# Optimization experiments

Hardware: AMD Instinct MI355X
Metric: run time of the kernel (lower is better)

## Reference

```python
import jax, jax.numpy as jnp
import numpy as np

# dims: batch B, tokens T, model_dim D, expert hidden H, experts E, top-k K
B, T, D, H, E, K = 4, 2048, 2048, 2048, 8, 2
CAP_FACTOR = 1.0
S = B * T
C = int(np.ceil(K * S / E * CAP_FACTOR))  # per-expert capacity = 2048


def setup_inputs() -> dict:
    key = jax.random.key(0)
    k0, k1, k2, k3 = jax.random.split(key, 4)
    x = jax.random.normal(k0, (B, T, D), dtype=jnp.float32)
    wg = jax.random.normal(k1, (D, E), dtype=jnp.float32) * (D ** -0.5)
    w1 = jax.random.normal(k2, (E, D, H), dtype=jnp.float32) * (D ** -0.5)
    b1 = jnp.zeros((E, H), dtype=jnp.float32)
    w2 = jax.random.normal(k3, (E, H, D), dtype=jnp.float32) * (H ** -0.5)
    b2 = jnp.zeros((E, D), dtype=jnp.float32)
    return {"x": x, "wg": wg, "w1": w1, "b1": b1, "w2": w2, "b2": b2}


def _moe(x, wg, w1, b1, w2, b2):
    xt = x.reshape(S, D)
    # --- top-k gating (deepspeed-style, gates normalized over selected k) ---
    gates = jax.nn.softmax(xt @ wg, axis=-1)            # [S,E]
    vals, idx = jax.lax.top_k(gates, K)                 # [S,K]
    vals = vals / jnp.sum(vals, axis=-1, keepdims=True)
    # --- capacity-aware slot assignment (slot j offset by counts of slots < j) ---
    m = jax.nn.one_hot(idx, E, dtype=jnp.int32).transpose(1, 0, 2)  # [K,S,E]
    within = jnp.cumsum(m, axis=1) - m                  # 0-based rank within expert per slot
    counts = jnp.sum(m, axis=1)                         # [K,E]
    offs = jnp.cumsum(counts, axis=0) - counts          # [K,E] offsets from earlier slots
    loc = jnp.sum((within + offs[:, None, :]) * m, axis=2)  # [K,S]
    eid = idx.T                                         # [K,S]
    valid = loc < C
    loc_c = jnp.minimum(loc, C - 1)
    # --- dispatch: scatter raw tokens into [E,C,D] expert buffers ---
    contrib = jnp.where(valid[..., None], xt[None, :, :], 0.0)   # [K,S,D]
    disp = jnp.zeros((E, C, D), x.dtype).at[eid, loc_c].add(contrib)
    # --- grouped expert FFN: relu(x @ W1 + b1) @ W2 + b2 ---
    h = jax.nn.relu(jnp.einsum('ecd,edh->ech', disp, w1) + b1[:, None, :])
    ye = jnp.einsum('ech,ehd->ecd', h, w2) + b2[:, None, :]
    # --- combine: gather expert outputs, weight by normalized gates ---
    gathered = ye[eid, loc_c]                           # [K,S,D]
    w = (vals.T * valid).astype(x.dtype)                # [K,S]
    out = jnp.einsum('ks,ksd->sd', w, gathered)
    return out.reshape(B, T, D)


def reference(x, wg, w1, b1, w2, b2):
    y = _moe(x, wg, w1, b1, w2, b2)                     # [B,T,D]
    return jax.nn.log_softmax(jnp.sum(y, axis=2), axis=1)  # [B,T]
```

## Files before the change

### kernel.cpp

```cpp
#include <hip/hip_runtime.h>
#include <math.h>

#define S_TOK 8192
#define DDIM 2048
#define HDIM 2048
#define NE 8
#define CAP 2048
#define NBATCH 4
#define TT 2048

typedef _Float16 f16;
typedef _Float16 f16x4 __attribute__((ext_vector_type(4)));
typedef _Float16 f16x8 __attribute__((ext_vector_type(8)));
typedef float f32x4 __attribute__((ext_vector_type(4)));

__global__ __launch_bounds__(256) void gating_kernel(const float* __restrict__ x,
                                                     const float* __restrict__ wg,
                                                     int* __restrict__ eid,
                                                     float* __restrict__ wts) {
  int wid = threadIdx.x >> 6;
  int lane = threadIdx.x & 63;
  int s = blockIdx.x * 4 + wid;
  const float4* x4 = (const float4*)x;
  const float4* wg4 = (const float4*)wg;
  double acc[8];
#pragma unroll
  for (int e = 0; e < 8; ++e) acc[e] = 0.0;
  for (int j = 0; j < 8; ++j) {
    int v = j * 64 + lane;
    float4 xv = x4[(size_t)s * 512 + v];
    const float4* wp = wg4 + (size_t)(v * 4) * 2;
#pragma unroll
    for (int ii = 0; ii < 4; ++ii) {
      float xs = (ii == 0) ? xv.x : (ii == 1) ? xv.y : (ii == 2) ? xv.z : xv.w;
      float4 g0 = wp[ii * 2];
      float4 g1 = wp[ii * 2 + 1];
      double xd = (double)xs;
      acc[0] += xd * (double)g0.x; acc[1] += xd * (double)g0.y;
      acc[2] += xd * (double)g0.z; acc[3] += xd * (double)g0.w;
      acc[4] += xd * (double)g1.x; acc[5] += xd * (double)g1.y;
      acc[6] += xd * (double)g1.z; acc[7] += xd * (double)g1.w;
    }
  }
#pragma unroll
  for (int e = 0; e < 8; ++e) {
    double v = acc[e];
    for (int off = 32; off > 0; off >>= 1) v += __shfl_down(v, off, 64);
    acc[e] = v;
  }
  if (lane == 0) {
    int e0 = 0; double l0 = acc[0];
    for (int e = 1; e < 8; ++e) if (acc[e] > l0) { l0 = acc[e]; e0 = e; }
    int e1 = -1; double l1 = -1e300;
    for (int e = 0; e < 8; ++e) if (e != e0 && acc[e] > l1) { l1 = acc[e]; e1 = e; }
    double pe = exp(l1 - l0);
    double inv = 1.0 / (1.0 + pe);
    eid[2 * s] = e0; eid[2 * s + 1] = e1;
    wts[2 * s] = (float)inv; wts[2 * s + 1] = (float)(pe * inv);
  }
}

__global__ __launch_bounds__(256) void w2s_kernel(const float* __restrict__ w2,
                                                  float* __restrict__ w2s) {
  int wid = threadIdx.x >> 6, lane = threadIdx.x & 63;
  int row = blockIdx.x * 4 + wid;
  const float4* w24 = (const float4*)w2;
  float acc = 0.f;
  for (int j = 0; j < 8; ++j) {
    float4 v = w24[(size_t)row * 512 + j * 64 + lane];
    acc += v.x + v.y + v.z + v.w;
  }
  for (int off = 32; off > 0; off >>= 1) acc += __shfl_down(acc, off, 64);
  if (lane == 0) w2s[row] = acc;
}

__global__ __launch_bounds__(64) void b2s_kernel(const float* __restrict__ b2,
                                                 float* __restrict__ b2s) {
  int e = blockIdx.x; int lane = threadIdx.x;
  float acc = 0.f;
  for (int j = 0; j < 32; ++j) acc += b2[e * 2048 + j * 64 + lane];
  for (int off = 32; off > 0; off >>= 1) acc += __shfl_down(acc, off, 64);
  if (lane == 0) b2s[e] = acc;
}

__global__ __launch_bounds__(256) void scan_kernel(const int* __restrict__ eid,
                                                   int* __restrict__ locb,
                                                   int* __restrict__ slot_token) {
  __shared__ int baseLds[2][8];
  __shared__ int wcnt[2][4][8];
  __shared__ int c0tmp[8];
  int tid = threadIdx.x, wid = tid >> 6, lane = tid & 63;
  if (tid < 8) c0tmp[tid] = 0;
  __syncthreads();
  {
    int cnt = 0;
    for (int r = 0; r < 32; ++r) {
      int s = r * 256 + tid;
      int e0 = eid[2 * s];
#pragma unroll
      for (int e = 0; e < 8; ++e) {
        unsigned long long bal = __ballot(e0 == e);
        if (lane == e) cnt += __popcll(bal);
      }
    }
    if (lane < 8) atomicAdd(&c0tmp[lane], cnt);
  }
  __syncthreads();
  if (tid < 8) { baseLds[0][tid] = 0; baseLds[1][tid] = c0tmp[tid]; }
  __syncthreads();
  unsigned long long lower = (lane == 0) ? 0ull : ((~0ull) >> (64 - lane));
  for (int r = 0; r < 32; ++r) {
    int s = r * 256 + tid;
    int e0 = eid[2 * s], e1 = eid[2 * s + 1];
    int rank0 = 0, rank1 = 0;
#pragma unroll
    for (int e = 0; e < 8; ++e) {
      unsigned long long bal0 = __ballot(e0 == e);
      unsigned long long bal1 = __ballot(e1 == e);
      if (e0 == e) rank0 = __popcll(bal0 & lower);
      if (e1 == e) rank1 = __popcll(bal1 & lower);
      if (lane == e) { wcnt[0][wid][e] = __popcll(bal0); wcnt[1][wid][e] = __popcll(bal1); }
    }
    __syncthreads();
    int loc0 = baseLds[0][e0] + rank0;
    int loc1 = baseLds[1][e1] + rank1;
    for (int w = 0; w < wid; ++w) { loc0 += wcnt[0][w][e0]; loc1 += wcnt[1][w][e1]; }
    locb[2 * s] = loc0; locb[2 * s + 1] = loc1;
    if (loc0 < CAP) slot_token[e0 * CAP + loc0] = s;
    if (loc1 < CAP) slot_token[e1 * CAP + loc1] = s;
    __syncthreads();
    if (tid < 16) {
      int k = tid >> 3, e = tid & 7;
      baseLds[k][e] += wcnt[k][0][e] + wcnt[k][1][e] + wcnt[k][2][e] + wcnt[k][3][e];
    }
    __syncthreads();
  }
}

__global__ __launch_bounds__(256) void abuild_kernel(const float* __restrict__ x,
                                                     const int* __restrict__ slot_token,
                                                     f16* __restrict__ A16) {
  int slot = blockIdx.x;
  int s = slot_token[slot];
  const float4* x4 = (const float4*)x + (size_t)s * 512;
  f16x4* out = (f16x4*)(A16 + (size_t)slot * DDIM);
#pragma unroll
  for (int i = 0; i < 2; ++i) {
    int v = i * 256 + threadIdx.x;
    float4 xv = x4[v];
    f16x4 h;
    h[0] = (f16)xv.x; h[1] = (f16)xv.y; h[2] = (f16)xv.z; h[3] = (f16)xv.w;
    out[v] = h;
  }
}

__global__ __launch_bounds__(256) void w1t_kernel(const float* __restrict__ w1,
                                                  f16* __restrict__ W1T) {
  __shared__ f16 tile[64 * 68];
  int b = blockIdx.x;
  int e = b >> 10; int rem = b & 1023;
  int d0 = (rem >> 5) << 6;
  int h0 = (rem & 31) << 6;
  const float4* src = (const float4*)w1;
#pragma unroll
  for (int i = 0; i < 4; ++i) {
    int linear = i * 256 + threadIdx.x;
    int r = linear >> 4, c4 = linear & 15;
    float4 v = src[((size_t)e * DDIM * HDIM + (size_t)(d0 + r) * HDIM + h0) / 4 + c4];
    int tb = r * 68 + c4 * 4;
    tile[tb + 0] = (f16)v.x; tile[tb + 1] = (f16)v.y;
    tile[tb + 2] = (f16)v.z; tile[tb + 3] = (f16)v.w;
  }
  __syncthreads();
#pragma unroll
  for (int i = 0; i < 4; ++i) {
    int linear = i * 256 + threadIdx.x;
    int hr = linear >> 4, dc4 = linear & 15;
    f16x4 o;
    o[0] = tile[(dc4 * 4 + 0) * 68 + hr];
    o[1] = tile[(dc4 * 4 + 1) * 68 + hr];
    o[2] = tile[(dc4 * 4 + 2) * 68 + hr];
    o[3] = tile[(dc4 * 4 + 3) * 68 + hr];
    *(f16x4*)(W1T + (size_t)e * HDIM * DDIM + (size_t)(h0 + hr) * DDIM + d0 + dc4 * 4) = o;
  }
}

__global__ __launch_bounds__(256) void gemm_kernel(const f16* __restrict__ A16,
                                                   const f16* __restrict__ W1T,
                                                   const float* __restrict__ b1,
                                                   const float* __restrict__ w2s,
                                                   float* __restrict__ zacc) {
  __shared__ __align__(16) f16 As[128 * 32];
  __shared__ __align__(16) f16 Bs[128 * 32];
  int tid = threadIdx.x;
  int wid = tid >> 6, lane = tid & 63;
  int cT = blockIdx.x, hT = blockIdx.y, e = blockIdx.z;
  int c0 = cT * 128, h0 = hT * 128;
  const f16* Abase = A16 + ((size_t)e * CAP + c0) * DDIM;
  const f16* Bbase = W1T + ((size_t)e * HDIM + h0) * DDIM;
  f32x4 acc[4][4];
#pragma unroll
  for (int i = 0; i < 4; ++i)
#pragma unroll
    for (int j = 0; j < 4; ++j) acc[i][j] = (f32x4){0.f, 0.f, 0.f, 0.f};
  int wm = (wid >> 1) * 64, wn = (wid & 1) * 64;
  int quad = lane >> 4, l15 = lane & 15;

  for (int k0 = 0; k0 < DDIM; k0 += 32) {
    __syncthreads();
#pragma unroll
    for (int i = 0; i < 2; ++i) {
      int off = (i * 256 + tid) * 8;
      int row = off >> 5, col = off & 31;
      *(uint4*)&As[off] = *(const uint4*)&Abase[(size_t)row * DDIM + k0 + col];
      *(uint4*)&Bs[off] = *(const uint4*)&Bbase[(size_t)row * DDIM + k0 + col];
    }
    __syncthreads();
    f16x8 af[4], bfr[4];
#pragma unroll
    for (int mt = 0; mt < 4; ++mt)
      af[mt] = *(const f16x8*)&As[(wm + mt * 16 + l15) * 32 + quad * 8];
#pragma unroll
    for (int nt = 0; nt < 4; ++nt)
      bfr[nt] = *(const f16x8*)&Bs[(wn + nt * 16 + l15) * 32 + quad * 8];
#pragma unroll
    for (int mt = 0; mt < 4; ++mt)
#pragma unroll
      for (int nt = 0; nt < 4; ++nt)
        acc[mt][nt] = __builtin_amdgcn_mfma_f32_16x16x32_f16(af[mt], bfr[nt], acc[mt][nt], 0, 0, 0);
  }
  float b1v[4], wsv[4];
#pragma unroll
  for (int nt = 0; nt < 4; ++nt) {
    int h = h0 + wn + nt * 16 + l15;
    b1v[nt] = b1[e * HDIM + h];
    wsv[nt] = w2s[e * HDIM + h];
  }
#pragma unroll
  for (int mt = 0; mt < 4; ++mt) {
    float pr[4];
#pragma unroll
    for (int r = 0; r < 4; ++r) {
      float t = 0.f;
#pragma unroll
      for (int nt = 0; nt < 4; ++nt) {
        float v = acc[mt][nt][r] + b1v[nt];
        t += (v > 0.f ? v : 0.f) * wsv[nt];
      }
      pr[r] = t;
    }
#pragma unroll
    for (int r = 0; r < 4; ++r)
#pragma unroll
      for (int off = 1; off < 16; off <<= 1) pr[r] += __shfl_xor(pr[r], off, 64);
    if (l15 == 0) {
      int m = c0 + wm + mt * 16 + quad * 4;
#pragma unroll
      for (int r = 0; r < 4; ++r) atomicAdd(&zacc[e * CAP + m + r], pr[r]);
    }
  }
}

__global__ __launch_bounds__(256) void combine_kernel(const int* __restrict__ eid,
                                                      const int* __restrict__ locb,
                                                      const float* __restrict__ wts,
                                                      const float* __restrict__ zacc,
                                                      const float* __restrict__ b2s,
                                                      float* __restrict__ z) {
  int s = blockIdx.x * 256 + threadIdx.x;
  float zz = 0.f;
#pragma unroll
  for (int k = 0; k < 2; ++k) {
    int e = eid[2 * s + k], loc = locb[2 * s + k];
    if (loc < CAP) zz += wts[2 * s + k] * (zacc[e * CAP + loc] + b2s[e]);
  }
  z[s] = zz;
}

__global__ __launch_bounds__(256) void lsm_kernel(const float* __restrict__ z,
                                                  float* __restrict__ out) {
  __shared__ float red[4];
  int b = blockIdx.x, tid = threadIdx.x;
  int wid = tid >> 6, lane = tid & 63;
  const float* zr = z + b * TT;
  float v[8];
  float mx = -1e30f;
#pragma unroll
  for (int i = 0; i < 8; ++i) { v[i] = zr[i * 256 + tid]; mx = fmaxf(mx, v[i]); }
  for (int off = 32; off > 0; off >>= 1) mx = fmaxf(mx, __shfl_xor(mx, off, 64));
  if (lane == 0) red[wid] = mx;
  __syncthreads();
  mx = fmaxf(fmaxf(red[0], red[1]), fmaxf(red[2], red[3]));
  float sum = 0.f;
#pragma unroll
  for (int i = 0; i < 8; ++i) sum += expf(v[i] - mx);
  for (int off = 32; off > 0; off >>= 1) sum += __shfl_xor(sum, off, 64);
  __syncthreads();
  if (lane == 0) red[wid] = sum;
  __syncthreads();
  sum = red[0] + red[1] + red[2] + red[3];
  float lse = mx + logf(sum);
#pragma unroll
  for (int i = 0; i < 8; ++i) out[b * TT + i * 256 + tid] = v[i] - lse;
}

extern "C" void kernel_launch(void* const* d_in, const int* in_sizes, int n_in,
                              void* d_out, int out_size, void* d_ws, size_t ws_size,
                              hipStream_t stream) {
  const float* x  = (const float*)d_in[0];
  const float* wg = (const float*)d_in[1];
  const float* w1 = (const float*)d_in[2];
  const float* b1 = (const float*)d_in[3];
  const float* w2 = (const float*)d_in[4];
  const float* b2 = (const float*)d_in[5];
  float* out = (float*)d_out;

  char* ws = (char*)d_ws;
  size_t off = 0;
  auto alloc = [&](size_t bytes) -> char* {
    char* p = ws + off;
    off += (bytes + 255) & ~(size_t)255;
    return p;
  };
  f16* A16 = (f16*)alloc((size_t)NE * CAP * DDIM * 2);
  f16* W1T = (f16*)alloc((size_t)NE * HDIM * DDIM * 2);
  float* w2s = (float*)alloc((size_t)NE * HDIM * 4);
  float* b2s = (float*)alloc(NE * 4);
  int* eid = (int*)alloc((size_t)S_TOK * 2 * 4);
  float* wts = (float*)alloc((size_t)S_TOK * 2 * 4);
  int* locb = (int*)alloc((size_t)S_TOK * 2 * 4);
  int* slot_token = (int*)alloc((size_t)NE * CAP * 4);
  float* zacc = (float*)alloc((size_t)NE * CAP * 4);
  float* z = (float*)alloc((size_t)S_TOK * 4);
  if (off > ws_size) return;

  hipMemsetAsync(slot_token, 0, NE * CAP * 4, stream);
  hipMemsetAsync(zacc, 0, NE * CAP * 4, stream);

  gating_kernel<<<S_TOK / 4, 256, 0, stream>>>(x, wg, eid, wts);
  w2s_kernel<<<NE * HDIM / 4, 256, 0, stream>>>(w2, w2s);
  b2s_kernel<<<NE, 64, 0, stream>>>(b2, b2s);
  scan_kernel<<<1, 256, 0, stream>>>(eid, locb, slot_token);
  abuild_kernel<<<NE * CAP, 256, 0, stream>>>(x, slot_token, A16);
  w1t_kernel<<<NE * 32 * 32, 256, 0, stream>>>(w1, W1T);
  gemm_kernel<<<dim3(CAP / 128, HDIM / 128, NE), 256, 0, stream>>>(A16, W1T, b1, w2s, zacc);
  combine_kernel<<<S_TOK / 256, 256, 0, stream>>>(eid, locb, wts, zacc, b2s, z);
  lsm_kernel<<<NBATCH, 256, 0, stream>>>(z, out);
}
```

Before: 650.7 us.

## Fuse prep kernels, drop memsets, use direct global-to-LDS loads in GEMM

Folds the workspace zeroing into the gating kernel and merges w1 transpose, w2/b2 row sums and the A16 build into a single prep launch. Combine and log-softmax are fused into one tail kernel. The GEMM now stages tiles with global_load_lds, bypassing registers, and remaps block IDs into 4x4 groups for L2 reuse. The w1 transpose tile is kept in fp32 with 8-wide f16 stores. This cuts launch count and staging overhead, but puts several unrelated changes together and leans on the direct-to-LDS builtin's layout matching the fragment reads.

```diff
diff --git a/kernel.cpp b/kernel.cpp
--- a/kernel.cpp
+++ b/kernel.cpp
@@ -14,10 +14,20 @@
 typedef _Float16 f16x8 __attribute__((ext_vector_type(8)));
 typedef float f32x4 __attribute__((ext_vector_type(4)));
 
+typedef __attribute__((address_space(1))) const void* gas_ptr;
+typedef __attribute__((address_space(3))) void* las_ptr;
+
 __global__ __launch_bounds__(256) void gating_kernel(const float* __restrict__ x,
                                                      const float* __restrict__ wg,
                                                      int* __restrict__ eid,
-                                                     float* __restrict__ wts) {
+                                                     float* __restrict__ wts,
+                                                     int* __restrict__ slot_token,
+                                                     float* __restrict__ zacc) {
+  if (blockIdx.x < 64) {
+    int i = blockIdx.x * 256 + threadIdx.x;
+    slot_token[i] = 0;
+    zacc[i] = 0.f;
+  }
   int wid = threadIdx.x >> 6;
   int lane = threadIdx.x & 63;
   int s = blockIdx.x * 4 + wid;
@@ -60,29 +70,6 @@
   }
 }
 
-__global__ __launch_bounds__(256) void w2s_kernel(const float* __restrict__ w2,
-                                                  float* __restrict__ w2s) {
-  int wid = threadIdx.x >> 6, lane = threadIdx.x & 63;
-  int row = blockIdx.x * 4 + wid;
-  const float4* w24 = (const float4*)w2;
-  float acc = 0.f;
-  for (int j = 0; j < 8; ++j) {
-    float4 v = w24[(size_t)row * 512 + j * 64 + lane];
-    acc += v.x + v.y + v.z + v.w;
-  }
-  for (int off = 32; off > 0; off >>= 1) acc += __shfl_down(acc, off, 64);
-  if (lane == 0) w2s[row] = acc;
-}
-
-__global__ __launch_bounds__(64) void b2s_kernel(const float* __restrict__ b2,
-                                                 float* __restrict__ b2s) {
-  int e = blockIdx.x; int lane = threadIdx.x;
-  float acc = 0.f;
-  for (int j = 0; j < 32; ++j) acc += b2[e * 2048 + j * 64 + lane];
-  for (int off = 32; off > 0; off >>= 1) acc += __shfl_down(acc, off, 64);
-  if (lane == 0) b2s[e] = acc;
-}
-
 __global__ __launch_bounds__(256) void scan_kernel(const int* __restrict__ eid,
                                                    int* __restrict__ locb,
                                                    int* __restrict__ slot_token) {
@@ -137,51 +124,80 @@
   }
 }
 
-__global__ __launch_bounds__(256) void abuild_kernel(const float* __restrict__ x,
-                                                     const int* __restrict__ slot_token,
-                                                     f16* __restrict__ A16) {
-  int slot = blockIdx.x;
-  int s = slot_token[slot];
-  const float4* x4 = (const float4*)x + (size_t)s * 512;
-  f16x4* out = (f16x4*)(A16 + (size_t)slot * DDIM);
-#pragma unroll
-  for (int i = 0; i < 2; ++i) {
-    int v = i * 256 + threadIdx.x;
-    float4 xv = x4[v];
-    f16x4 h;
-    h[0] = (f16)xv.x; h[1] = (f16)xv.y; h[2] = (f16)xv.z; h[3] = (f16)xv.w;
-    out[v] = h;
-  }
-}
-
-__global__ __launch_bounds__(256) void w1t_kernel(const float* __restrict__ w1,
-                                                  f16* __restrict__ W1T) {
-  __shared__ f16 tile[64 * 68];
-  int b = blockIdx.x;
-  int e = b >> 10; int rem = b & 1023;
-  int d0 = (rem >> 5) << 6;
-  int h0 = (rem & 31) << 6;
-  const float4* src = (const float4*)w1;
-#pragma unroll
-  for (int i = 0; i < 4; ++i) {
-    int linear = i * 256 + threadIdx.x;
-    int r = linear >> 4, c4 = linear & 15;
-    float4 v = src[((size_t)e * DDIM * HDIM + (size_t)(d0 + r) * HDIM + h0) / 4 + c4];
-    int tb = r * 68 + c4 * 4;
-    tile[tb + 0] = (f16)v.x; tile[tb + 1] = (f16)v.y;
-    tile[tb + 2] = (f16)v.z; tile[tb + 3] = (f16)v.w;
-  }
-  __syncthreads();
-#pragma unroll
-  for (int i = 0; i < 4; ++i) {
-    int linear = i * 256 + threadIdx.x;
-    int hr = linear >> 4, dc4 = linear & 15;
-    f16x4 o;
-    o[0] = tile[(dc4 * 4 + 0) * 68 + hr];
-    o[1] = tile[(dc4 * 4 + 1) * 68 + hr];
-    o[2] = tile[(dc4 * 4 + 2) * 68 + hr];
-    o[3] = tile[(dc4 * 4 + 3) * 68 + hr];
-    *(f16x4*)(W1T + (size_t)e * HDIM * DDIM + (size_t)(h0 + hr) * DDIM + d0 + dc4 * 4) = o;
+#define W1T_BLOCKS 8192
+#define W2S_BLOCKS 4096
+#define ABUILD_BASE (W1T_BLOCKS + W2S_BLOCKS + 1)
+__global__ __launch_bounds__(256) void prep_kernel(const float* __restrict__ w1,
+                                                   const float* __restrict__ w2,
+                                                   const float* __restrict__ b2,
+                                                   const float* __restrict__ x,
+                                                   const int* __restrict__ slot_token,
+                                                   f16* __restrict__ W1T,
+                                                   float* __restrict__ w2s,
+                                                   float* __restrict__ b2s,
+                                                   f16* __restrict__ A16) {
+  __shared__ float tile[64 * 65];
+  int bid = blockIdx.x, tid = threadIdx.x;
+  if (bid >= ABUILD_BASE) {
+    int slot = bid - ABUILD_BASE;
+    int s = slot_token[slot];
+    const float4* x4 = (const float4*)x + (size_t)s * 512;
+    f16x4* outp = (f16x4*)(A16 + (size_t)slot * DDIM);
+#pragma unroll
+    for (int i = 0; i < 2; ++i) {
+      int v = i * 256 + tid;
+      float4 xv = x4[v];
+      f16x4 h;
+      h[0] = (f16)xv.x; h[1] = (f16)xv.y; h[2] = (f16)xv.z; h[3] = (f16)xv.w;
+      outp[v] = h;
+    }
+    return;
+  }
+  if (bid < W1T_BLOCKS) {
+    int e = bid >> 10, rem = bid & 1023;
+    int d0 = (rem >> 5) << 6;
+    int h0 = (rem & 31) << 6;
+    const float* w1e = w1 + (size_t)e * DDIM * HDIM;
+#pragma unroll
+    for (int i = 0; i < 4; ++i) {
+      int linear = i * 256 + tid;
+      int r = linear >> 4, c4 = linear & 15;
+      float4 v = *(const float4*)(w1e + (size_t)(d0 + r) * HDIM + h0 + c4 * 4);
+      float* t = &tile[r * 65 + c4 * 4];
+      t[0] = v.x; t[1] = v.y; t[2] = v.z; t[3] = v.w;
+    }
+    __syncthreads();
+    f16* W1Te = W1T + (size_t)e * HDIM * DDIM;
+#pragma unroll
+    for (int i = 0; i < 2; ++i) {
+      int linear = i * 256 + tid;
+      int hr = linear >> 3, l8 = linear & 7;
+      f16x8 o;
+#pragma unroll
+      for (int j = 0; j < 8; ++j) o[j] = (f16)tile[(l8 * 8 + j) * 65 + hr];
+      *(f16x8*)(W1Te + (size_t)(h0 + hr) * DDIM + d0 + l8 * 8) = o;
+    }
+    return;
+  }
+  if (bid < W1T_BLOCKS + W2S_BLOCKS) {
+    int wid = tid >> 6, lane = tid & 63;
+    int row = (bid - W1T_BLOCKS) * 4 + wid;
+    const float4* w24 = (const float4*)w2;
+    float acc = 0.f;
+    for (int j = 0; j < 8; ++j) {
+      float4 v = w24[(size_t)row * 512 + j * 64 + lane];
+      acc += v.x + v.y + v.z + v.w;
+    }
+    for (int off = 32; off > 0; off >>= 1) acc += __shfl_down(acc, off, 64);
+    if (lane == 0) w2s[row] = acc;
+    return;
+  }
+  {
+    int e = tid >> 5, l32 = tid & 31;
+    float acc = 0.f;
+    for (int j = 0; j < 64; ++j) acc += b2[e * 2048 + j * 32 + l32];
+    for (int off = 16; off > 0; off >>= 1) acc += __shfl_down(acc, off, 32);
+    if (l32 == 0) b2s[e] = acc;
   }
 }
 
@@ -194,7 +210,12 @@
   __shared__ __align__(16) f16 Bs[128 * 32];
   int tid = threadIdx.x;
   int wid = tid >> 6, lane = tid & 63;
-  int cT = blockIdx.x, hT = blockIdx.y, e = blockIdx.z;
+  int bid = blockIdx.x;
+  int e = bid >> 8;
+  int r = bid & 255;
+  int st = r >> 4, wi = r & 15;
+  int cT = (st >> 2) * 4 + (wi >> 2);
+  int hT = (st & 3) * 4 + (wi & 3);
   int c0 = cT * 128, h0 = hT * 128;
   const f16* Abase = A16 + ((size_t)e * CAP + c0) * DDIM;
   const f16* Bbase = W1T + ((size_t)e * HDIM + h0) * DDIM;
@@ -206,15 +227,19 @@
   int wm = (wid >> 1) * 64, wn = (wid & 1) * 64;
   int quad = lane >> 4, l15 = lane & 15;
 
+  const f16* Aln = Abase + (size_t)(wid * 32 + (lane >> 2)) * DDIM + (lane & 3) * 8;
+  const f16* Bln = Bbase + (size_t)(wid * 32 + (lane >> 2)) * DDIM + (lane & 3) * 8;
+  f16* ldsA0 = &As[wid * 1024];
+  f16* ldsA1 = &As[wid * 1024 + 512];
+  f16* ldsB0 = &Bs[wid * 1024];
+  f16* ldsB1 = &Bs[wid * 1024 + 512];
+
   for (int k0 = 0; k0 < DDIM; k0 += 32) {
     __syncthreads();
-#pragma unroll
-    for (int i = 0; i < 2; ++i) {
-      int off = (i * 256 + tid) * 8;
-      int row = off >> 5, col = off & 31;
-      *(uint4*)&As[off] = *(const uint4*)&Abase[(size_t)row * DDIM + k0 + col];
-      *(uint4*)&Bs[off] = *(const uint4*)&Bbase[(size_t)row * DDIM + k0 + col];
-    }
+    __builtin_amdgcn_global_load_lds((gas_ptr)(Aln + k0), (las_ptr)ldsA0, 16, 0, 0);
+    __builtin_amdgcn_global_load_lds((gas_ptr)(Aln + k0 + 16 * DDIM), (las_ptr)ldsA1, 16, 0, 0);
+    __builtin_amdgcn_global_load_lds((gas_ptr)(Bln + k0), (las_ptr)ldsB0, 16, 0, 0);
+    __builtin_amdgcn_global_load_lds((gas_ptr)(Bln + k0 + 16 * DDIM), (las_ptr)ldsB1, 16, 0, 0);
     __syncthreads();
     f16x8 af[4], bfr[4];
 #pragma unroll
@@ -240,53 +265,50 @@
   for (int mt = 0; mt < 4; ++mt) {
     float pr[4];
 #pragma unroll
-    for (int r = 0; r < 4; ++r) {
+    for (int rr = 0; rr < 4; ++rr) {
       float t = 0.f;
 #pragma unroll
       for (int nt = 0; nt < 4; ++nt) {
-        float v = acc[mt][nt][r] + b1v[nt];
+        float v = acc[mt][nt][rr] + b1v[nt];
         t += (v > 0.f ? v : 0.f) * wsv[nt];
       }
-      pr[r] = t;
-    }
-#pragma unroll
-    for (int r = 0; r < 4; ++r)
-#pragma unroll
-      for (int off = 1; off < 16; off <<= 1) pr[r] += __shfl_xor(pr[r], off, 64);
+      pr[rr] = t;
+    }
+#pragma unroll
+    for (int rr = 0; rr < 4; ++rr)
+#pragma unroll
+      for (int off = 1; off < 16; off <<= 1) pr[rr] += __shfl_xor(pr[rr], off, 64);
     if (l15 == 0) {
       int m = c0 + wm + mt * 16 + quad * 4;
 #pragma unroll
-      for (int r = 0; r < 4; ++r) atomicAdd(&zacc[e * CAP + m + r], pr[r]);
-    }
-  }
-}
-
-__global__ __launch_bounds__(256) void combine_kernel(const int* __restrict__ eid,
-                                                      const int* __restrict__ locb,
-                                                      const float* __restrict__ wts,
-                                                      const float* __restrict__ zacc,
-                                                      const float* __restrict__ b2s,
-                                                      float* __restrict__ z) {
-  int s = blockIdx.x * 256 + threadIdx.x;
-  float zz = 0.f;
-#pragma unroll
-  for (int k = 0; k < 2; ++k) {
-    int e = eid[2 * s + k], loc = locb[2 * s + k];
-    if (loc < CAP) zz += wts[2 * s + k] * (zacc[e * CAP + loc] + b2s[e]);
-  }
-  z[s] = zz;
-}
-
-__global__ __launch_bounds__(256) void lsm_kernel(const float* __restrict__ z,
-                                                  float* __restrict__ out) {
+      for (int rr = 0; rr < 4; ++rr) atomicAdd(&zacc[e * CAP + m + rr], pr[rr]);
+    }
+  }
+}
+
+__global__ __launch_bounds__(256) void tail_kernel(const int* __restrict__ eid,
+                                                   const int* __restrict__ locb,
+                                                   const float* __restrict__ wts,
+                                                   const float* __restrict__ zacc,
+                                                   const float* __restrict__ b2s,
+                                                   float* __restrict__ out) {
   __shared__ float red[4];
   int b = blockIdx.x, tid = threadIdx.x;
   int wid = tid >> 6, lane = tid & 63;
-  const float* zr = z + b * TT;
   float v[8];
   float mx = -1e30f;
 #pragma unroll
-  for (int i = 0; i < 8; ++i) { v[i] = zr[i * 256 + tid]; mx = fmaxf(mx, v[i]); }
+  for (int i = 0; i < 8; ++i) {
+    int s = b * TT + i * 256 + tid;
+    float zz = 0.f;
+#pragma unroll
+    for (int k = 0; k < 2; ++k) {
+      int e = eid[2 * s + k], loc = locb[2 * s + k];
+      if (loc < CAP) zz += wts[2 * s + k] * (zacc[e * CAP + loc] + b2s[e]);
+    }
+    v[i] = zz;
+    mx = fmaxf(mx, zz);
+  }
   for (int off = 32; off > 0; off >>= 1) mx = fmaxf(mx, __shfl_xor(mx, off, 64));
   if (lane == 0) red[wid] = mx;
   __syncthreads();
@@ -331,19 +353,12 @@
   int* locb = (int*)alloc((size_t)S_TOK * 2 * 4);
   int* slot_token = (int*)alloc((size_t)NE * CAP * 4);
   float* zacc = (float*)alloc((size_t)NE * CAP * 4);
-  float* z = (float*)alloc((size_t)S_TOK * 4);
   if (off > ws_size) return;
 
-  hipMemsetAsync(slot_token, 0, NE * CAP * 4, stream);
-  hipMemsetAsync(zacc, 0, NE * CAP * 4, stream);
-
-  gating_kernel<<<S_TOK / 4, 256, 0, stream>>>(x, wg, eid, wts);
-  w2s_kernel<<<NE * HDIM / 4, 256, 0, stream>>>(w2, w2s);
-  b2s_kernel<<<NE, 64, 0, stream>>>(b2, b2s);
+  gating_kernel<<<S_TOK / 4, 256, 0, stream>>>(x, wg, eid, wts, slot_token, zacc);
   scan_kernel<<<1, 256, 0, stream>>>(eid, locb, slot_token);
-  abuild_kernel<<<NE * CAP, 256, 0, stream>>>(x, slot_token, A16);
-  w1t_kernel<<<NE * 32 * 32, 256, 0, stream>>>(w1, W1T);
-  gemm_kernel<<<dim3(CAP / 128, HDIM / 128, NE), 256, 0, stream>>>(A16, W1T, b1, w2s, zacc);
-  combine_kernel<<<S_TOK / 256, 256, 0, stream>>>(eid, locb, wts, zacc, b2s, z);
-  lsm_kernel<<<NBATCH, 256, 0, stream>>>(z, out);
-}
+  prep_kernel<<<ABUILD_BASE + NE * CAP, 256, 0, stream>>>(w1, w2, b2, x, slot_token,
+                                                          W1T, w2s, b2s, A16);
+  gemm_kernel<<<NE * 256, 256, 0, stream>>>(A16, W1T, b1, w2s, zacc);
+  tail_kernel<<<NBATCH, 256, 0, stream>>>(eid, locb, wts, zacc, b2s, out);
+}
```

Measured after the change: 618.7 us. -4.9%, faster.
